# Optimization experiments

Hardware: AMD Instinct MI355X
Metric: run time of the kernel (lower is better)

## Reference

```python
import jax, jax.numpy as jnp
import numpy as np

N_TOKENS = 8192
D_MODEL = 1024
N_EXPERT = 8
TOP_K = 2
D_HIDDEN = 4 * D_MODEL


def setup_inputs() -> dict:
    key = jax.random.key(0)
    ks = jax.random.split(key, 7)
    s_in = 1.0 / np.sqrt(D_MODEL)
    s_hid = 1.0 / np.sqrt(D_HIDDEN)
    return {
        "inp": jax.random.normal(ks[0], (N_TOKENS, D_MODEL), dtype=jnp.float32),
        "gate_w": jax.random.normal(ks[1], (D_MODEL, N_EXPERT), dtype=jnp.float32) * s_in,
        "gate_b": jnp.zeros((N_EXPERT,), dtype=jnp.float32),
        "w1": jax.random.normal(ks[2], (N_EXPERT, D_MODEL, D_HIDDEN), dtype=jnp.float32) * s_in,
        "b1": jnp.zeros((N_EXPERT, D_HIDDEN), dtype=jnp.float32),
        "w2": jax.random.normal(ks[3], (N_EXPERT, D_HIDDEN, D_MODEL), dtype=jnp.float32) * s_hid,
        "b2": jnp.zeros((N_EXPERT, D_MODEL), dtype=jnp.float32),
    }


def reference(inp, gate_w, gate_b, w1, b1, w2, b2):
    # NaiveGate: linear logits -> top_k -> softmax over the selected k logits
    logits = inp @ gate_w + gate_b                      # [N, E]
    top_vals, top_idx = jax.lax.top_k(logits, TOP_K)    # [N, K]
    gate_score = jax.nn.softmax(top_vals, axis=-1)      # [N, K]

    # Dispatch/combine: y[n] = sum_k score[n,k] * expert_{idx[n,k]}(x[n]).
    # Loop over the small fixed expert set; mask-weighted accumulate replaces
    # the scatter / grouped-GEMM / gather of the original (same math).
    y = jnp.zeros_like(inp)
    for e in range(N_EXPERT):
        h = jax.nn.gelu(inp @ w1[e] + b1[e])             # [N, H]
        o = h @ w2[e] + b2[e]                            # [N, D]
        w_e = jnp.sum(gate_score * (top_idx == e), axis=-1)  # [N]
        y = y + w_e[:, None] * o
    return y
```

## Files before the change

### kernel.cpp

```cpp
#include <hip/hip_runtime.h>
#include <hip/hip_bf16.h>

#define NT 8192
#define DM 1024
#define NE 8
#define DH 4096
#define NP (NT * 2)

typedef __attribute__((ext_vector_type(8))) __bf16 bf16x8;
typedef __attribute__((ext_vector_type(4))) float f32x4;

__device__ __forceinline__ ushort f2bf(float f) {
  unsigned int x = __float_as_uint(f);
  unsigned int r = (x + 0x7fffu + ((x >> 16) & 1u)) >> 16;
  return (ushort)r;
}

__device__ __forceinline__ float gelu_fast(float x) {
  float x2 = x * x;
  float t = __builtin_fmaf(x2, 0.044715f, 1.0f);
  float m = x * t * 2.3025851f;
  m = fminf(m, 126.0f);
  float p = __builtin_amdgcn_exp2f(m);
  return x * p * __builtin_amdgcn_rcpf(p + 1.0f);
}

__device__ __forceinline__ void async_copy16(const void* gsrc, void* ldst) {
  __builtin_amdgcn_global_load_lds(
      (const __attribute__((address_space(1))) void*)gsrc,
      (__attribute__((address_space(3))) void*)ldst, 16, 0, 0);
}

__global__ __launch_bounds__(256) void fused_pre_kernel(
    const float* __restrict__ w1, const float* __restrict__ w2,
    ushort* __restrict__ w1t, ushort* __restrict__ w2t,
    const float* __restrict__ inp, const float* __restrict__ gw,
    const float* __restrict__ gb, ushort* __restrict__ inp_bf,
    int* __restrict__ counts, int* __restrict__ tok_list,
    float* __restrict__ scale_list, float* __restrict__ y) {
  __shared__ ushort tileT[64][72];
  const int b = blockIdx.x;

  if (b < 16384) {
    const int which = b >> 13;
    const int rem = b & 8191;
    const int e = rem >> 10;
    const int t = rem & 1023;
    const float* src;
    ushort* dst;
    int R, C, c0, r0;
    if (which == 0) {
      src = w1 + (size_t)e * DM * DH; dst = w1t + (size_t)e * DM * DH;
      R = DM; C = DH; c0 = (t & 63) * 64; r0 = (t >> 6) * 64;
    } else {
      src = w2 + (size_t)e * DM * DH; dst = w2t + (size_t)e * DM * DH;
      R = DH; C = DM; c0 = (t & 15) * 64; r0 = (t >> 4) * 64;
    }
    const int tx = threadIdx.x & 15, ty = threadIdx.x >> 4;
#pragma unroll
    for (int i = 0; i < 4; i++) {
      int r = ty + i * 16;
      float4 v = *(const float4*)(src + (size_t)(r0 + r) * C + c0 + tx * 4);
      tileT[tx * 4 + 0][r] = f2bf(v.x);
      tileT[tx * 4 + 1][r] = f2bf(v.y);
      tileT[tx * 4 + 2][r] = f2bf(v.z);
      tileT[tx * 4 + 3][r] = f2bf(v.w);
    }
    __syncthreads();
#pragma unroll
    for (int i = 0; i < 4; i++) {
      int c = ty + i * 16;
      *(ushort4*)(dst + (size_t)(c0 + c) * R + r0 + tx * 4) = *(const ushort4*)(&tileT[c][tx * 4]);
    }
  } else if (b < 18432) {
    const int wave = threadIdx.x >> 6, lane = threadIdx.x & 63;
    const int token = (b - 16384) * 4 + wave;
    const float* x = inp + (size_t)token * DM;
    ushort* xb = inp_bf + (size_t)token * DM;
    float acc[NE];
#pragma unroll
    for (int e = 0; e < NE; e++) acc[e] = 0.f;
#pragma unroll
    for (int j = 0; j < 16; j++) {
      int idx = j * 64 + lane;
      float xv = x[idx];
      xb[idx] = f2bf(xv);
      const float4* g = (const float4*)(gw + (size_t)idx * NE);
      float4 g0 = g[0], g1 = g[1];
      acc[0] += xv * g0.x; acc[1] += xv * g0.y; acc[2] += xv * g0.z; acc[3] += xv * g0.w;
      acc[4] += xv * g1.x; acc[5] += xv * g1.y; acc[6] += xv * g1.z; acc[7] += xv * g1.w;
    }
#pragma unroll
    for (int e = 0; e < NE; e++) {
      for (int off = 32; off; off >>= 1) acc[e] += __shfl_xor(acc[e], off, 64);
    }
    if (lane == 0) {
      float v[NE];
#pragma unroll
      for (int e = 0; e < NE; e++) v[e] = acc[e] + gb[e];
      int i0 = 0; float b0 = v[0];
#pragma unroll
      for (int e = 1; e < NE; e++) if (v[e] > b0) { b0 = v[e]; i0 = e; }
      int i1 = -1; float b1v = -INFINITY;
#pragma unroll
      for (int e = 0; e < NE; e++) if (e != i0 && v[e] > b1v) { b1v = v[e]; i1 = e; }
      float s1 = 1.f / (1.f + __expf(b0 - b1v));
      float s0 = 1.f - s1;
      int p0 = atomicAdd(&counts[i0], 1);
      tok_list[i0 * NT + p0] = token;
      scale_list[i0 * NT + p0] = s0;
      int p1 = atomicAdd(&counts[i1], 1);
      tok_list[i1 * NT + p1] = token;
      scale_list[i1 * NT + p1] = s1;
    }
  } else {
    const int idx = b - 18432;
    float4* dst = (float4*)(y + (size_t)idx * 4096);
    f32x4 z = {0.f, 0.f, 0.f, 0.f};
#pragma unroll
    for (int j = 0; j < 4; j++)
      ((f32x4*)dst)[j * 256 + threadIdx.x] = z;
  }
}


#define STAGE_TILE(base)                                      \
  do {                                                        \
    async_copy16(aP0, (char*)(base) + wv * 1024);             \
    async_copy16(aP1, (char*)(base) + 4096 + wv * 1024);      \
    async_copy16(bP0, (char*)(base) + 8192 + wv * 1024);      \
    async_copy16(bP1, (char*)(base) + 12288 + wv * 1024);     \
    aP0 += 32; aP1 += 32; bP0 += 32; bP1 += 32;               \
  } while (0)

__global__ __launch_bounds__(256) void gemm1_kernel(
    const ushort* __restrict__ xbf, const ushort* __restrict__ w1t,
    const float* __restrict__ b1, const int* __restrict__ tok_list,
    const int* __restrict__ counts, ushort* __restrict__ hbuf) {
  const int b = blockIdx.x;
  const int e = b & 7;
  const int idx = b >> 3;
  const int mTile = idx & 63;
  const int nTile = idx >> 6;
  int off = 0;
  for (int i = 0; i < e; i++) off += counts[i];
  const int cnt = counts[e];
  if (mTile * 128 >= cnt) return;

  __shared__ __attribute__((aligned(128))) char ldsB[49152];

  const int t = threadIdx.x;
  const int lane = t & 63, wv = t >> 6;
  const int wm = wv & 1, wn = wv >> 1;

  const int sr = t >> 2;
  const int sc = (((t & 3) ^ ((sr >> 1) & 3)) * 8);
  int gi0 = mTile * 128 + sr;      if (gi0 >= cnt) gi0 = cnt - 1;
  int gi1 = mTile * 128 + 64 + sr; if (gi1 >= cnt) gi1 = cnt - 1;
  const int tok0 = tok_list[e * NT + gi0];
  const int tok1 = tok_list[e * NT + gi1];
  const ushort* aP0 = xbf + (size_t)tok0 * DM + sc;
  const ushort* aP1 = xbf + (size_t)tok1 * DM + sc;
  const ushort* bP0 = w1t + ((size_t)e * DH + nTile * 128 + sr) * DM + sc;
  const ushort* bP1 = bP0 + (size_t)64 * DM;

  f32x4 zero = {0.f, 0.f, 0.f, 0.f};
  f32x4 acc[4][4];
#pragma unroll
  for (int i = 0; i < 4; i++)
#pragma unroll
    for (int j = 0; j < 4; j++) acc[i][j] = zero;

  const int quad = lane >> 4, lc = lane & 15;
  const int rq = quad ^ ((lc >> 1) & 3);

  auto compute = [&](const char* buf) {
    const char* A_ = buf;
    const char* B_ = buf + 8192;
    bf16x8 af[4], bfr[4];
#pragma unroll
    for (int mi = 0; mi < 4; mi++) {
      int row = wm * 64 + mi * 16 + lc;
      af[mi] = *(const bf16x8*)(A_ + row * 64 + rq * 16);
    }
#pragma unroll
    for (int ni = 0; ni < 4; ni++) {
      int row = wn * 64 + ni * 16 + lc;
      bfr[ni] = *(const bf16x8*)(B_ + row * 64 + rq * 16);
    }
#pragma unroll
    for (int mi = 0; mi < 4; mi++)
#pragma unroll
      for (int ni = 0; ni < 4; ni++)
        acc[mi][ni] = __builtin_amdgcn_mfma_f32_16x16x32_bf16(af[mi], bfr[ni], acc[mi][ni], 0, 0, 0);
  };

  const int NIT = DM / 32;
  STAGE_TILE(ldsB);
  STAGE_TILE(ldsB + 16384);
  int cur = 0;
  for (int tt = 0; tt < NIT - 1; ++tt) {
    asm volatile("s_waitcnt vmcnt(4)" ::: "memory");
    __builtin_amdgcn_s_barrier();
    if (tt + 2 < NIT) {
      int nx = cur + 2; if (nx >= 3) nx -= 3;
      STAGE_TILE(ldsB + nx * 16384);
    }
    compute(ldsB + cur * 16384);
    cur = (cur == 2) ? 0 : cur + 1;
  }
  asm volatile("s_waitcnt vmcnt(0)" ::: "memory");
  __builtin_amdgcn_s_barrier();
  compute(ldsB + cur * 16384);

  float bias[4];
#pragma unroll
  for (int ni = 0; ni < 4; ni++)
    bias[ni] = b1[(size_t)e * DH + nTile * 128 + wn * 64 + ni * 16 + lc];

#pragma unroll
  for (int mi = 0; mi < 4; mi++) {
#pragma unroll
    for (int r = 0; r < 4; r++) {
      int lr = wm * 64 + mi * 16 + quad * 4 + r;
      int gi = mTile * 128 + lr;
      if (gi < cnt) {
        ushort* hrow = hbuf + (size_t)(off + gi) * DH + nTile * 128 + wn * 64 + lc;
#pragma unroll
        for (int ni = 0; ni < 4; ni++) {
          float v = acc[mi][ni][r] + bias[ni];
          hrow[ni * 16] = f2bf(gelu_fast(v));
        }
      }
    }
  }
}

__global__ __launch_bounds__(256) void gemm2_kernel(
    const ushort* __restrict__ hbuf, const ushort* __restrict__ w2t,
    const float* __restrict__ b2, const int* __restrict__ tok_list,
    const float* __restrict__ scale_list, const int* __restrict__ counts,
    float* __restrict__ y) {
  const int b = blockIdx.x;
  const int e = b & 7;
  const int idx = b >> 3;
  const int nTile = idx & 7;
  const int mTile = idx >> 3;
  int off = 0;
  for (int i = 0; i < e; i++) off += counts[i];
  const int cnt = counts[e];
  if (mTile * 128 >= cnt) return;

  __shared__ __attribute__((aligned(128))) char ldsB[49152];

  const int t = threadIdx.x;
  const int lane = t & 63, wv = t >> 6;
  const int wm = wv & 1, wn = wv >> 1;

  const int sr = t >> 2;
  const int sc = (((t & 3) ^ ((sr >> 1) & 3)) * 8);
  int gi0 = mTile * 128 + sr;      if (gi0 >= cnt) gi0 = cnt - 1;
  int gi1 = mTile * 128 + 64 + sr; if (gi1 >= cnt) gi1 = cnt - 1;
  const ushort* aP0 = hbuf + (size_t)(off + gi0) * DH + sc;
  const ushort* aP1 = hbuf + (size_t)(off + gi1) * DH + sc;
  const ushort* bP0 = w2t + ((size_t)e * DM + nTile * 128 + sr) * DH + sc;
  const ushort* bP1 = bP0 + (size_t)64 * DH;

  f32x4 zero = {0.f, 0.f, 0.f, 0.f};
  f32x4 acc[4][4];
#pragma unroll
  for (int i = 0; i < 4; i++)
#pragma unroll
    for (int j = 0; j < 4; j++) acc[i][j] = zero;

  const int quad = lane >> 4, lc = lane & 15;
  const int rq = quad ^ ((lc >> 1) & 3);

  auto compute = [&](const char* buf) {
    const char* A_ = buf;
    const char* B_ = buf + 8192;
    bf16x8 af[4], bfr[4];
#pragma unroll
    for (int mi = 0; mi < 4; mi++) {
      int row = wm * 64 + mi * 16 + lc;
      af[mi] = *(const bf16x8*)(A_ + row * 64 + rq * 16);
    }
#pragma unroll
    for (int ni = 0; ni < 4; ni++) {
      int row = wn * 64 + ni * 16 + lc;
      bfr[ni] = *(const bf16x8*)(B_ + row * 64 + rq * 16);
    }
#pragma unroll
    for (int mi = 0; mi < 4; mi++)
#pragma unroll
      for (int ni = 0; ni < 4; ni++)
        acc[mi][ni] = __builtin_amdgcn_mfma_f32_16x16x32_bf16(af[mi], bfr[ni], acc[mi][ni], 0, 0, 0);
  };

  const int NIT = DH / 32;
  STAGE_TILE(ldsB);
  STAGE_TILE(ldsB + 16384);
  int cur = 0;
  for (int tt = 0; tt < NIT - 1; ++tt) {
    asm volatile("s_waitcnt vmcnt(4)" ::: "memory");
    __builtin_amdgcn_s_barrier();
    if (tt + 2 < NIT) {
      int nx = cur + 2; if (nx >= 3) nx -= 3;
      STAGE_TILE(ldsB + nx * 16384);
    }
    compute(ldsB + cur * 16384);
    cur = (cur == 2) ? 0 : cur + 1;
  }
  asm volatile("s_waitcnt vmcnt(0)" ::: "memory");
  __builtin_amdgcn_s_barrier();
  compute(ldsB + cur * 16384);

  float bias[4];
#pragma unroll
  for (int ni = 0; ni < 4; ni++)
    bias[ni] = b2[(size_t)e * DM + nTile * 128 + wn * 64 + ni * 16 + lc];

#pragma unroll
  for (int mi = 0; mi < 4; mi++) {
#pragma unroll
    for (int r = 0; r < 4; r++) {
      int lr = wm * 64 + mi * 16 + quad * 4 + r;
      int gi = mTile * 128 + lr;
      if (gi < cnt) {
        int tok = tok_list[e * NT + gi];
        float s = scale_list[e * NT + gi];
        float* yrow = y + (size_t)tok * DM + nTile * 128 + wn * 64 + lc;
#pragma unroll
        for (int ni = 0; ni < 4; ni++) {
          float v = (acc[mi][ni][r] + bias[ni]) * s;
          unsafeAtomicAdd(&yrow[ni * 16], v);
        }
      }
    }
  }
}

extern "C" void kernel_launch(void* const* d_in, const int* in_sizes, int n_in,
                              void* d_out, int out_size, void* d_ws, size_t ws_size,
                              hipStream_t stream) {
  const float* inp = (const float*)d_in[0];
  const float* gw  = (const float*)d_in[1];
  const float* gb  = (const float*)d_in[2];
  const float* w1  = (const float*)d_in[3];
  const float* b1  = (const float*)d_in[4];
  const float* w2  = (const float*)d_in[5];
  const float* b2  = (const float*)d_in[6];
  float* y = (float*)d_out;

  char* ws = (char*)d_ws;
  ushort* inp_bf = (ushort*)ws;              ws += (size_t)NT * DM * 2;
  ushort* w1t    = (ushort*)ws;              ws += (size_t)NE * DH * DM * 2;
  ushort* w2t    = (ushort*)ws;              ws += (size_t)NE * DM * DH * 2;
  ushort* hbuf   = (ushort*)ws;              ws += (size_t)NP * DH * 2;
  int*    tok_list   = (int*)ws;             ws += (size_t)NE * NT * 4;
  float*  scale_list = (float*)ws;           ws += (size_t)NE * NT * 4;
  int*    counts     = (int*)ws;             ws += 256;

  hipMemsetAsync(counts, 0, 256, stream);

  fused_pre_kernel<<<20480, 256, 0, stream>>>(w1, w2, w1t, w2t, inp, gw, gb,
                                              inp_bf, counts, tok_list, scale_list, y);
  gemm1_kernel<<<NE * 32 * 64, 256, 0, stream>>>(inp_bf, w1t, b1, tok_list, counts, hbuf);
  gemm2_kernel<<<NE * 8 * 64, 256, 0, stream>>>(hbuf, w2t, b2, tok_list, scale_list, counts, y);
}
```

Before: 905.6 us.

## Drop weight transpose; transpose B tiles in registers inside GEMM kernels

The pre-kernel now only converts the fp32 expert weights to bf16 in their original row-major layout instead of transposing them through shared memory. Each GEMM kernel loads B tiles with ordinary global loads into registers, interleaves pairs of K rows by bit-packing, and writes them into LDS in the swizzled k-contiguous layout the MFMA fragments expect. The main loop is unrolled by two with separate register buffers for each stage. This removes the strided transpose writes in preprocessing, but adds register pressure, extra LDS store instructions and lgkmcnt waits to the GEMM inner loop.

```diff
diff --git a/kernel.cpp b/kernel.cpp
--- a/kernel.cpp
+++ b/kernel.cpp
@@ -33,44 +33,26 @@
 
 __global__ __launch_bounds__(256) void fused_pre_kernel(
     const float* __restrict__ w1, const float* __restrict__ w2,
-    ushort* __restrict__ w1t, ushort* __restrict__ w2t,
+    ushort* __restrict__ w1b, ushort* __restrict__ w2b,
     const float* __restrict__ inp, const float* __restrict__ gw,
     const float* __restrict__ gb, ushort* __restrict__ inp_bf,
     int* __restrict__ counts, int* __restrict__ tok_list,
     float* __restrict__ scale_list, float* __restrict__ y) {
-  __shared__ ushort tileT[64][72];
   const int b = blockIdx.x;
 
   if (b < 16384) {
-    const int which = b >> 13;
-    const int rem = b & 8191;
-    const int e = rem >> 10;
-    const int t = rem & 1023;
     const float* src;
     ushort* dst;
-    int R, C, c0, r0;
-    if (which == 0) {
-      src = w1 + (size_t)e * DM * DH; dst = w1t + (size_t)e * DM * DH;
-      R = DM; C = DH; c0 = (t & 63) * 64; r0 = (t >> 6) * 64;
-    } else {
-      src = w2 + (size_t)e * DM * DH; dst = w2t + (size_t)e * DM * DH;
-      R = DH; C = DM; c0 = (t & 15) * 64; r0 = (t >> 4) * 64;
-    }
-    const int tx = threadIdx.x & 15, ty = threadIdx.x >> 4;
-#pragma unroll
-    for (int i = 0; i < 4; i++) {
-      int r = ty + i * 16;
-      float4 v = *(const float4*)(src + (size_t)(r0 + r) * C + c0 + tx * 4);
-      tileT[tx * 4 + 0][r] = f2bf(v.x);
-      tileT[tx * 4 + 1][r] = f2bf(v.y);
-      tileT[tx * 4 + 2][r] = f2bf(v.z);
-      tileT[tx * 4 + 3][r] = f2bf(v.w);
-    }
-    __syncthreads();
-#pragma unroll
-    for (int i = 0; i < 4; i++) {
-      int c = ty + i * 16;
-      *(ushort4*)(dst + (size_t)(c0 + c) * R + r0 + tx * 4) = *(const ushort4*)(&tileT[c][tx * 4]);
+    if (b < 8192) { src = w1 + (size_t)b * 4096; dst = w1b + (size_t)b * 4096; }
+    else          { src = w2 + (size_t)(b - 8192) * 4096; dst = w2b + (size_t)(b - 8192) * 4096; }
+    const float4* s4 = (const float4*)src;
+    ushort4* d4 = (ushort4*)dst;
+    const int t = threadIdx.x;
+#pragma unroll
+    for (int j = 0; j < 4; j++) {
+      float4 v = s4[t + j * 256];
+      ushort4 o = { f2bf(v.x), f2bf(v.y), f2bf(v.z), f2bf(v.w) };
+      d4[t + j * 256] = o;
     }
   } else if (b < 18432) {
     const int wave = threadIdx.x >> 6, lane = threadIdx.x & 63;
@@ -124,17 +106,39 @@
 }
 
 
-#define STAGE_TILE(base)                                      \
-  do {                                                        \
-    async_copy16(aP0, (char*)(base) + wv * 1024);             \
-    async_copy16(aP1, (char*)(base) + 4096 + wv * 1024);      \
-    async_copy16(bP0, (char*)(base) + 8192 + wv * 1024);      \
-    async_copy16(bP1, (char*)(base) + 12288 + wv * 1024);     \
-    aP0 += 32; aP1 += 32; bP0 += 32; bP1 += 32;               \
+#define STAGE_A(base)                                      \
+  do {                                                     \
+    async_copy16(aP0, (char*)(base) + wv * 1024);          \
+    async_copy16(aP1, (char*)(base) + 4096 + wv * 1024);   \
+    aP0 += 32; aP1 += 32;                                  \
   } while (0)
 
+#define LOAD_B(ra, rb, LDB)                                \
+  do {                                                     \
+    ra = *(const uint4*)(bSrc);                            \
+    rb = *(const uint4*)(bSrc + (LDB));                    \
+    bSrc += (size_t)32 * (LDB);                            \
+  } while (0)
+
+#define WRITE_B(Breg, ra, rb)                                                  \
+  do {                                                                         \
+    uint d0 = (ra.x & 0xffffu) | (rb.x << 16);                                 \
+    uint d1 = (ra.x >> 16)     | (rb.x & 0xffff0000u);                         \
+    uint d2 = (ra.y & 0xffffu) | (rb.y << 16);                                 \
+    uint d3 = (ra.y >> 16)     | (rb.y & 0xffff0000u);                         \
+    uint d4 = (ra.z & 0xffffu) | (rb.z << 16);                                 \
+    uint d5 = (ra.z >> 16)     | (rb.z & 0xffff0000u);                         \
+    uint d6 = (ra.w & 0xffffu) | (rb.w << 16);                                 \
+    uint d7 = (ra.w >> 16)     | (rb.w & 0xffff0000u);                         \
+    char* bb = (char*)(Breg) + wbBase;                                         \
+    *(uint*)(bb + wbOff0) = d0;  *(uint*)(bb + wbOff0 + 64) = d1;              \
+    *(uint*)(bb + wbOff1) = d2;  *(uint*)(bb + wbOff1 + 64) = d3;              \
+    *(uint*)(bb + wbOff2) = d4;  *(uint*)(bb + wbOff2 + 64) = d5;              \
+    *(uint*)(bb + wbOff3) = d6;  *(uint*)(bb + wbOff3 + 64) = d7;              \
+  } while (0)
+
 __global__ __launch_bounds__(256) void gemm1_kernel(
-    const ushort* __restrict__ xbf, const ushort* __restrict__ w1t,
+    const ushort* __restrict__ xbf, const ushort* __restrict__ w1b,
     const float* __restrict__ b1, const int* __restrict__ tok_list,
     const int* __restrict__ counts, ushort* __restrict__ hbuf) {
   const int b = blockIdx.x;
@@ -161,8 +165,17 @@
   const int tok1 = tok_list[e * NT + gi1];
   const ushort* aP0 = xbf + (size_t)tok0 * DM + sc;
   const ushort* aP1 = xbf + (size_t)tok1 * DM + sc;
-  const ushort* bP0 = w1t + ((size_t)e * DH + nTile * 128 + sr) * DM + sc;
-  const ushort* bP1 = bP0 + (size_t)64 * DM;
+
+  const int br = t & 15;
+  const int bg = t >> 4;
+  const ushort* bSrc = w1b + (size_t)e * DM * DH + (size_t)(2 * br) * DH + nTile * 128 + bg * 8;
+  const int wbBase = 512 * bg + 4 * (br & 3);
+  const int s_ = br >> 2;
+  const int wbOff0 = 16 * (s_ ^ 0) + 0;
+  const int wbOff1 = 16 * (s_ ^ 1) + 128;
+  const int wbOff2 = 16 * (s_ ^ 2) + 256;
+  const int wbOff3 = 16 * (s_ ^ 3) + 384;
+  uint4 raA, rbA, raB, rbB;
 
   f32x4 zero = {0.f, 0.f, 0.f, 0.f};
   f32x4 acc[4][4];
@@ -196,20 +209,36 @@
   };
 
   const int NIT = DM / 32;
-  STAGE_TILE(ldsB);
-  STAGE_TILE(ldsB + 16384);
+  STAGE_A(ldsB);           LOAD_B(raA, rbA, DH);
+  STAGE_A(ldsB + 16384);   LOAD_B(raB, rbB, DH);
   int cur = 0;
-  for (int tt = 0; tt < NIT - 1; ++tt) {
+  for (int tt = 0; tt < NIT - 2; tt += 2) {
     asm volatile("s_waitcnt vmcnt(4)" ::: "memory");
+    WRITE_B(ldsB + cur * 16384 + 8192, raA, rbA);
+    asm volatile("s_waitcnt lgkmcnt(0)" ::: "memory");
     __builtin_amdgcn_s_barrier();
-    if (tt + 2 < NIT) {
-      int nx = cur + 2; if (nx >= 3) nx -= 3;
-      STAGE_TILE(ldsB + nx * 16384);
-    }
+    { int nx = cur + 2; if (nx >= 3) nx -= 3;
+      STAGE_A(ldsB + nx * 16384);  LOAD_B(raA, rbA, DH); }
+    compute(ldsB + cur * 16384);
+    cur = (cur == 2) ? 0 : cur + 1;
+    asm volatile("s_waitcnt vmcnt(4)" ::: "memory");
+    WRITE_B(ldsB + cur * 16384 + 8192, raB, rbB);
+    asm volatile("s_waitcnt lgkmcnt(0)" ::: "memory");
+    __builtin_amdgcn_s_barrier();
+    { int nx = cur + 2; if (nx >= 3) nx -= 3;
+      STAGE_A(ldsB + nx * 16384);  LOAD_B(raB, rbB, DH); }
     compute(ldsB + cur * 16384);
     cur = (cur == 2) ? 0 : cur + 1;
   }
+  asm volatile("s_waitcnt vmcnt(4)" ::: "memory");
+  WRITE_B(ldsB + cur * 16384 + 8192, raA, rbA);
+  asm volatile("s_waitcnt lgkmcnt(0)" ::: "memory");
+  __builtin_amdgcn_s_barrier();
+  compute(ldsB + cur * 16384);
+  cur = (cur == 2) ? 0 : cur + 1;
   asm volatile("s_waitcnt vmcnt(0)" ::: "memory");
+  WRITE_B(ldsB + cur * 16384 + 8192, raB, rbB);
+  asm volatile("s_waitcnt lgkmcnt(0)" ::: "memory");
   __builtin_amdgcn_s_barrier();
   compute(ldsB + cur * 16384);
 
@@ -237,7 +266,7 @@
 }
 
 __global__ __launch_bounds__(256) void gemm2_kernel(
-    const ushort* __restrict__ hbuf, const ushort* __restrict__ w2t,
+    const ushort* __restrict__ hbuf, const ushort* __restrict__ w2b,
     const float* __restrict__ b2, const int* __restrict__ tok_list,
     const float* __restrict__ scale_list, const int* __restrict__ counts,
     float* __restrict__ y) {
@@ -263,8 +292,17 @@
   int gi1 = mTile * 128 + 64 + sr; if (gi1 >= cnt) gi1 = cnt - 1;
   const ushort* aP0 = hbuf + (size_t)(off + gi0) * DH + sc;
   const ushort* aP1 = hbuf + (size_t)(off + gi1) * DH + sc;
-  const ushort* bP0 = w2t + ((size_t)e * DM + nTile * 128 + sr) * DH + sc;
-  const ushort* bP1 = bP0 + (size_t)64 * DH;
+
+  const int br = t & 15;
+  const int bg = t >> 4;
+  const ushort* bSrc = w2b + (size_t)e * DH * DM + (size_t)(2 * br) * DM + nTile * 128 + bg * 8;
+  const int wbBase = 512 * bg + 4 * (br & 3);
+  const int s_ = br >> 2;
+  const int wbOff0 = 16 * (s_ ^ 0) + 0;
+  const int wbOff1 = 16 * (s_ ^ 1) + 128;
+  const int wbOff2 = 16 * (s_ ^ 2) + 256;
+  const int wbOff3 = 16 * (s_ ^ 3) + 384;
+  uint4 raA, rbA, raB, rbB;
 
   f32x4 zero = {0.f, 0.f, 0.f, 0.f};
   f32x4 acc[4][4];
@@ -298,20 +336,36 @@
   };
 
   const int NIT = DH / 32;
-  STAGE_TILE(ldsB);
-  STAGE_TILE(ldsB + 16384);
+  STAGE_A(ldsB);           LOAD_B(raA, rbA, DM);
+  STAGE_A(ldsB + 16384);   LOAD_B(raB, rbB, DM);
   int cur = 0;
-  for (int tt = 0; tt < NIT - 1; ++tt) {
+  for (int tt = 0; tt < NIT - 2; tt += 2) {
     asm volatile("s_waitcnt vmcnt(4)" ::: "memory");
+    WRITE_B(ldsB + cur * 16384 + 8192, raA, rbA);
+    asm volatile("s_waitcnt lgkmcnt(0)" ::: "memory");
     __builtin_amdgcn_s_barrier();
-    if (tt + 2 < NIT) {
-      int nx = cur + 2; if (nx >= 3) nx -= 3;
-      STAGE_TILE(ldsB + nx * 16384);
-    }
+    { int nx = cur + 2; if (nx >= 3) nx -= 3;
+      STAGE_A(ldsB + nx * 16384);  LOAD_B(raA, rbA, DM); }
+    compute(ldsB + cur * 16384);
+    cur = (cur == 2) ? 0 : cur + 1;
+    asm volatile("s_waitcnt vmcnt(4)" ::: "memory");
+    WRITE_B(ldsB + cur * 16384 + 8192, raB, rbB);
+    asm volatile("s_waitcnt lgkmcnt(0)" ::: "memory");
+    __builtin_amdgcn_s_barrier();
+    { int nx = cur + 2; if (nx >= 3) nx -= 3;
+      STAGE_A(ldsB + nx * 16384);  LOAD_B(raB, rbB, DM); }
     compute(ldsB + cur * 16384);
     cur = (cur == 2) ? 0 : cur + 1;
   }
+  asm volatile("s_waitcnt vmcnt(4)" ::: "memory");
+  WRITE_B(ldsB + cur * 16384 + 8192, raA, rbA);
+  asm volatile("s_waitcnt lgkmcnt(0)" ::: "memory");
+  __builtin_amdgcn_s_barrier();
+  compute(ldsB + cur * 16384);
+  cur = (cur == 2) ? 0 : cur + 1;
   asm volatile("s_waitcnt vmcnt(0)" ::: "memory");
+  WRITE_B(ldsB + cur * 16384 + 8192, raB, rbB);
+  asm volatile("s_waitcnt lgkmcnt(0)" ::: "memory");
   __builtin_amdgcn_s_barrier();
   compute(ldsB + cur * 16384);
 
@@ -354,8 +408,8 @@
 
   char* ws = (char*)d_ws;
   ushort* inp_bf = (ushort*)ws;              ws += (size_t)NT * DM * 2;
-  ushort* w1t    = (ushort*)ws;              ws += (size_t)NE * DH * DM * 2;
-  ushort* w2t    = (ushort*)ws;              ws += (size_t)NE * DM * DH * 2;
+  ushort* w1b    = (ushort*)ws;              ws += (size_t)NE * DM * DH * 2;
+  ushort* w2b    = (ushort*)ws;              ws += (size_t)NE * DH * DM * 2;
   ushort* hbuf   = (ushort*)ws;              ws += (size_t)NP * DH * 2;
   int*    tok_list   = (int*)ws;             ws += (size_t)NE * NT * 4;
   float*  scale_list = (float*)ws;           ws += (size_t)NE * NT * 4;
@@ -363,8 +417,8 @@
 
   hipMemsetAsync(counts, 0, 256, stream);
 
-  fused_pre_kernel<<<20480, 256, 0, stream>>>(w1, w2, w1t, w2t, inp, gw, gb,
+  fused_pre_kernel<<<20480, 256, 0, stream>>>(w1, w2, w1b, w2b, inp, gw, gb,
                                               inp_bf, counts, tok_list, scale_list, y);
-  gemm1_kernel<<<NE * 32 * 64, 256, 0, stream>>>(inp_bf, w1t, b1, tok_list, counts, hbuf);
-  gemm2_kernel<<<NE * 8 * 64, 256, 0, stream>>>(hbuf, w2t, b2, tok_list, scale_list, counts, y);
-}
+  gemm1_kernel<<<NE * 32 * 64, 256, 0, stream>>>(inp_bf, w1b, b1, tok_list, counts, hbuf);
+  gemm2_kernel<<<NE * 8 * 64, 256, 0, stream>>>(hbuf, w2b, b2, tok_list, scale_list, counts, y);
+}
```

After: 1.126 ms. 24.4% more time.
